# Kernel optimization log

Measured on AMD Instinct MI355X. Metric: run time of the kernel, lower is better.

Reference implementation:

```python
import jax, jax.numpy as jnp
import numpy as np

N_NODES = 100000


def setup_inputs() -> dict:
    key = jax.random.key(0)
    k1, k2, k3 = jax.random.split(key, 3)
    x = jax.random.normal(k1, (N_NODES, 128), dtype=jnp.float32)
    edge_index = jax.random.randint(k2, (2, 1600000), 0, N_NODES, dtype=jnp.int64)
    # TAGConv K=1 linear weight: maps concat([x, Ax]) (2*in) -> out; stored as [(K+1)*in, out]
    W = (jax.random.normal(k3, (256, 128), dtype=jnp.float32) / np.sqrt(256.0)).astype(jnp.float32)
    return {"x": x, "edge_index": edge_index, "W": W}


def reference(x, edge_index, W):
    src, dst = edge_index[0], edge_index[1]
    n = x.shape[0]
    ones = jnp.ones(src.shape[0], dtype=x.dtype)
    # gcn_norm without self-loops: degree from edge weights scattered at target
    deg = jax.ops.segment_sum(ones, dst, num_segments=n)
    dis = jnp.where(deg > 0, jax.lax.rsqrt(jnp.where(deg > 0, deg, 1.0)), 0.0)
    norm = dis[src] * dis[dst]  # [E]
    # message passing: out[dst] += norm * x[src]
    msgs = x[src] * norm[:, None]  # [E, in]
    agg = jax.ops.segment_sum(msgs, dst, num_segments=n)  # [N, in]
    h = jnp.concatenate([x, agg], axis=1)  # [N, 2*in]
    return h @ W  # [N, out]
```

## Files before the change

### kernel.cpp

```cpp
#include <hip/hip_runtime.h>


#define GCN_F 128
#define BINCAP 9216
#define EPACK_ROWS 14112

typedef __attribute__((ext_vector_type(8))) short frag_ab;
typedef __attribute__((ext_vector_type(4))) float frag_cd;

__device__ __forceinline__ unsigned short f2bf(float f) {
    unsigned int u = __float_as_uint(f);
    unsigned int r = (u + 0x7FFFu + ((u >> 16) & 1u)) >> 16;
    return (unsigned short)r;
}

__device__ __forceinline__ int detect_is32(const unsigned int* ei32, int* s_is32) {
    if (threadIdx.x == 0) *s_is32 = 0;
    __syncthreads();
    unsigned int v = 0;
    for (int i = threadIdx.x; i < 2048; i += blockDim.x) v |= ei32[2 * i + 1];
    if (v != 0u) atomicOr(s_is32, 1);
    __syncthreads();
    return *s_is32;
}

__device__ __forceinline__ int load_idx(const int* ei, int is32, long long pos) {
    if (is32) return ei[pos];
    return ((const int2*)ei)[pos].x;
}

__device__ __forceinline__ void xbf_store(const float4* x4, char* xb, int xs, int g) {
    int r = g >> 5, q = g & 31;
    float4 v = x4[(long long)r * 32 + q];
    ushort4 o;
    o.x = f2bf(v.x); o.y = f2bf(v.y); o.z = f2bf(v.z); o.w = f2bf(v.w);
    *(ushort4*)(xb + ((unsigned)r << xs) + q * 8) = o;
}

__global__ __launch_bounds__(256) void bscatter_kernel(const int* __restrict__ ei,
                                                       int* __restrict__ gcur,
                                                       unsigned int* __restrict__ epack,
                                                       int E, int EB,
                                                       const float* __restrict__ W,
                                                       unsigned short* __restrict__ wt,
                                                       const float4* __restrict__ x4,
                                                       char* __restrict__ xb,
                                                       int xs, int g0, int Ntot) {
    int tid = threadIdx.x;
    if ((int)blockIdx.x >= EB + 128) {
        int g = g0 + (blockIdx.x - (EB + 128)) * 256 + tid;
        if (g < Ntot * 32) xbf_store(x4, xb, xs, g);
        return;
    }
    if ((int)blockIdx.x >= EB) {
        int c = blockIdx.x - EB;
        wt[c * 256 + tid] = f2bf(W[tid * GCN_F + c]);
        return;
    }
    __shared__ int h[4][256];
    __shared__ int lcur[256];
    __shared__ int s_is32;
    int wv = tid >> 6;
    for (int i = tid; i < 1024; i += 256) ((int*)h)[i] = 0;
    int is32 = detect_is32((const unsigned int*)ei, &s_is32);
    int base = blockIdx.x * 4096;
    unsigned int pk[16];
    int bn[16];
#pragma unroll
    for (int j = 0; j < 16; ++j) {
        int e = base + j * 256 + tid;
        bn[j] = -1;
        pk[j] = 0;
        if (e < E) {
            int src = load_idx(ei, is32, e);
            int dst = load_idx(ei, is32, (long long)E + e);
            pk[j] = (unsigned int)src | (((unsigned int)dst & 511u) << 17);
            bn[j] = dst >> 9;
            atomicAdd(&h[wv][bn[j]], 1);
        }
    }
    __syncthreads();
    {
        int cnt = h[0][tid] + h[1][tid] + h[2][tid] + h[3][tid];
        if (cnt > 0) {
            int run = atomicAdd(&gcur[tid], cnt);
            if (run + cnt > BINCAP) run = BINCAP - cnt;
            lcur[tid] = tid * BINCAP + run;
        }
    }
    __syncthreads();
#pragma unroll
    for (int j = 0; j < 16; ++j) {
        if (bn[j] >= 0) {
            int pos = atomicAdd(&lcur[bn[j]], 1);
            epack[pos] = pk[j];
        }
    }
}

__global__ __launch_bounds__(512) void fcsr_kernel(const unsigned int* __restrict__ epack,
                                                   const int* __restrict__ gcur,
                                                   int* __restrict__ start,
                                                   float* __restrict__ dis,
                                                   int* __restrict__ ebuf,
                                                   int N) {
    __shared__ int stmp[256];
    __shared__ int s_base, s_total;
    __shared__ int lh[512];
    __shared__ int sc[512];
    int c = blockIdx.x;
    int tid = threadIdx.x;
    int v0 = 0;
    if (tid < 256) {
        v0 = min(gcur[tid], BINCAP);
        stmp[tid] = v0;
    }
    lh[tid] = 0;
    __syncthreads();
    for (int off = 1; off < 256; off <<= 1) {
        int t = (tid < 256 && tid >= off) ? stmp[tid - off] : 0;
        __syncthreads();
        if (tid < 256) stmp[tid] += t;
        __syncthreads();
    }
    if (tid == c) s_base = stmp[tid] - v0;
    if (tid == 255) s_total = stmp[255];
    __syncthreads();
    int b = c * BINCAP;
    int e = b + min(gcur[c], BINCAP);
    for (int i = b + tid; i < e; i += 512) {
        atomicAdd(&lh[(epack[i] >> 17) & 511u], 1);
    }
    __syncthreads();
    sc[tid] = lh[tid];
    __syncthreads();
    for (int off = 1; off < 512; off <<= 1) {
        int t = (tid >= off) ? sc[tid - off] : 0;
        __syncthreads();
        sc[tid] += t;
        __syncthreads();
    }
    int d = lh[tid];
    int gs = s_base + sc[tid] - d;
    int node = c * 512 + tid;
    if (node < N) {
        start[node] = gs;
        dis[node] = (d > 0) ? rsqrtf((float)d) : 0.0f;
    }
    __syncthreads();
    sc[tid] = gs;
    if (c == 0 && tid == 0) start[N] = s_total;
    __syncthreads();
    for (int i = b + tid; i < e; i += 512) {
        unsigned int v = epack[i];
        int pos = atomicAdd(&sc[(v >> 17) & 511u], 1);
        ebuf[pos] = (int)(v & 0x1FFFFu);
    }
}

__global__ __launch_bounds__(256) void xbf_lo_kernel(const float4* __restrict__ x4,
                                                     char* __restrict__ xb, int xs) {
    int g = blockIdx.x * 256 + threadIdx.x;
    if (g >= EPACK_ROWS * 32) return;
    xbf_store(x4, xb, xs, g);
}

__global__ __launch_bounds__(256) void gather_kernel(const char* __restrict__ xb, int xs,
                                                     char* __restrict__ aggb,
                                                     const int* __restrict__ ebuf,
                                                     const int* __restrict__ start,
                                                     const float* __restrict__ dis,
                                                     int N) {
    int node = blockIdx.x * 4 + (threadIdx.x >> 6);
    if (node >= N) return;
    int lane = threadIdx.x & 63;
    int slot = lane >> 4;
    unsigned int subb = (lane & 15) * 16;
    int s = start[node];
    int d = start[node + 1] - s;
    float nd = dis[node];
    float acc[8];
#pragma unroll
    for (int i = 0; i < 8; ++i) acc[i] = 0.0f;

    for (int base = 0; base < d; base += 64) {
        int cn = min(64, d - base);
        int eid = 0; float dv = 0.0f;
        if (lane < cn) {
            eid = ebuf[s + base + lane];
            dv = dis[eid];
        }
        int njj = (cn + 3) >> 2;
#pragma unroll 4
        for (int j = 0; j < njj; ++j) {
            int tt = 4 * j + slot;
            int src = __shfl(eid, tt);
            float f = __shfl(dv, tt);
            uint4 u = *(const uint4*)(xb + (((unsigned)src << xs) + subb));
            acc[0] += f * __uint_as_float(u.x << 16);
            acc[1] += f * __uint_as_float(u.x);
            acc[2] += f * __uint_as_float(u.y << 16);
            acc[3] += f * __uint_as_float(u.y);
            acc[4] += f * __uint_as_float(u.z << 16);
            acc[5] += f * __uint_as_float(u.z);
            acc[6] += f * __uint_as_float(u.w << 16);
            acc[7] += f * __uint_as_float(u.w);
        }
    }
#pragma unroll
    for (int i = 0; i < 8; ++i) {
        acc[i] += __shfl_xor(acc[i], 16);
        acc[i] += __shfl_xor(acc[i], 32);
    }
    if (slot == 0) {
        uint4 o;
        o.x = (unsigned int)f2bf(acc[0] * nd) | ((unsigned int)f2bf(acc[1] * nd) << 16);
        o.y = (unsigned int)f2bf(acc[2] * nd) | ((unsigned int)f2bf(acc[3] * nd) << 16);
        o.z = (unsigned int)f2bf(acc[4] * nd) | ((unsigned int)f2bf(acc[5] * nd) << 16);
        o.w = (unsigned int)f2bf(acc[6] * nd) | ((unsigned int)f2bf(acc[7] * nd) << 16);
        *(uint4*)(aggb + (((unsigned)node << 9) + 256 + subb)) = o;
    }
}

#define GEMM_BM 128
__global__ __launch_bounds__(256) void gemm_mfma_kernel(
        const char* __restrict__ xb, int xs,
        const char* aggb,
        const unsigned short* __restrict__ wt,
        float* out, int N) {
    int wave = threadIdx.x >> 6;
    int lane = threadIdx.x & 63;
    int lr = lane & 15;
    int kh = lane >> 4;
    int rowbase = blockIdx.x * GEMM_BM + wave * 32;

    frag_cd acc[2][8];
#pragma unroll
    for (int rt = 0; rt < 2; ++rt)
#pragma unroll
        for (int ct = 0; ct < 8; ++ct) acc[rt][ct] = (frag_cd)0.0f;

#pragma unroll
    for (int ks = 0; ks < 8; ++ks) {
        frag_ab a[2];
#pragma unroll
        for (int rt = 0; rt < 2; ++rt) {
            int r = rowbase + rt * 16 + lr;
            r = min(r, N - 1);
            const char* ap = (ks < 4)
                ? (xb   + (((unsigned)r << xs) + (unsigned)(ks * 64 + kh * 16)))
                : (aggb + (((unsigned)r << 9) + (unsigned)(256 + (ks - 4) * 64 + kh * 16)));
            a[rt] = *(const frag_ab*)ap;
        }
#pragma unroll
        for (int ct = 0; ct < 8; ++ct) {
            int c = ct * 16 + lr;
            frag_ab b = *(const frag_ab*)(wt + c * 256 + ks * 32 + kh * 8);
#pragma unroll
            for (int rt = 0; rt < 2; ++rt) {
                acc[rt][ct] = __builtin_amdgcn_mfma_f32_16x16x32_bf16(a[rt], b, acc[rt][ct], 0, 0, 0);
            }
        }
    }
#pragma unroll
    for (int rt = 0; rt < 2; ++rt) {
#pragma unroll
        for (int ct = 0; ct < 8; ++ct) {
#pragma unroll
            for (int reg = 0; reg < 4; ++reg) {
                int r = rowbase + rt * 16 + kh * 4 + reg;
                if (r < N) out[r * GCN_F + ct * 16 + lr] = acc[rt][ct][reg];
            }
        }
    }
}

extern "C" void kernel_launch(void* const* d_in, const int* in_sizes, int n_in,
                              void* d_out, int out_size, void* d_ws, size_t ws_size,
                              hipStream_t stream) {
    const float* x  = (const float*)d_in[0];
    const int*   ei = (const int*)d_in[1];
    const float* W  = (const float*)d_in[2];
    float* out = (float*)d_out;

    const int N = in_sizes[0] / GCN_F;
    const int E = in_sizes[1] / 2;

    char* ws = (char*)d_ws;
    int*   gcur  = (int*)ws;
    float* dis   = (float*)(ws + 8192);
    int*   start = (int*)(ws + 408192);
    int*   ebuf  = (int*)(ws + 808208);
    unsigned short* wt = (unsigned short*)(ws + 7208208);
    char*  xb_ws = ws + 7274496;

    unsigned int* epack = (unsigned int*)d_out;
    char*         aggb  = (char*)d_out;

    const size_t WS_NEED = 7274496 + (size_t)N * 256;
    const bool bigws = ws_size >= WS_NEED;

    char* xb = bigws ? xb_ws : (char*)d_out;
    int   xs = bigws ? 8 : 9;
    int g0 = bigws ? 0 : EPACK_ROWS * 32;
    int XR = (N * 32 - g0 + 255) / 256;

    const int CB = (N + 511) / 512;
    const int EB = (E + 4095) / 4096;

    hipMemsetAsync(d_ws, 0, 1024, stream);

    bscatter_kernel<<<EB + 128 + XR, 256, 0, stream>>>(
        ei, gcur, epack, E, EB, W, wt, (const float4*)x, xb, xs, g0, N);
    fcsr_kernel<<<CB, 512, 0, stream>>>(epack, gcur, start, dis, ebuf, N);
    if (!bigws) {
        xbf_lo_kernel<<<(EPACK_ROWS * 32 + 255) / 256, 256, 0, stream>>>(
            (const float4*)x, xb, xs);
    }
    gather_kernel<<<(N + 3) / 4, 256, 0, stream>>>(xb, xs, aggb, ebuf, start, dis, N);
    gemm_mfma_kernel<<<(N + GEMM_BM - 1) / GEMM_BM, 256, 0, stream>>>(
        xb, xs, aggb, wt, out, N);
}
```

Measured before the change: 160.8 us.

## Vectorize edge loads, drop second LDS atomic pass, gather two nodes per wave

```diff
diff --git a/kernel.cpp b/kernel.cpp
--- a/kernel.cpp
+++ b/kernel.cpp
@@ -58,44 +58,84 @@
         return;
     }
     __shared__ int h[4][256];
-    __shared__ int lcur[256];
     __shared__ int s_is32;
     int wv = tid >> 6;
     for (int i = tid; i < 1024; i += 256) ((int*)h)[i] = 0;
     int is32 = detect_is32((const unsigned int*)ei, &s_is32);
     int base = blockIdx.x * 4096;
     unsigned int pk[16];
-    int bn[16];
+    int bn[16], rk[16];
+#pragma unroll
+    for (int j = 0; j < 16; ++j) bn[j] = -1;
+
+#define BS_PROC(j, sv, dv_)                                          \
+    {                                                                \
+        unsigned int ud = (unsigned int)(dv_);                       \
+        pk[j] = (unsigned int)(sv) | ((ud & 511u) << 17);            \
+        int b_ = (int)(ud >> 9);                                     \
+        bn[j] = b_;                                                  \
+        rk[j] = atomicAdd(&h[wv][b_], 1);                            \
+    }
+
+    if (is32 && ((E & 3) == 0)) {
+#pragma unroll
+        for (int jj = 0; jj < 4; ++jj) {
+            int e0 = base + jj * 1024 + tid * 4;
+            if (e0 < E) {
+                int4 s4 = *(const int4*)(ei + e0);
+                int4 d4 = *(const int4*)(ei + (size_t)E + e0);
+                int js = jj * 4;
+                BS_PROC(js + 0, s4.x, d4.x); BS_PROC(js + 1, s4.y, d4.y);
+                BS_PROC(js + 2, s4.z, d4.z); BS_PROC(js + 3, s4.w, d4.w);
+            }
+        }
+    } else if (!is32) {
+#pragma unroll
+        for (int jj = 0; jj < 8; ++jj) {
+            int e0 = base + jj * 512 + tid * 2;
+            if (e0 + 1 < E) {
+                int4 s2 = *(const int4*)((const int2*)ei + e0);
+                int4 d2 = *(const int4*)((const int2*)ei + (size_t)E + e0);
+                BS_PROC(jj * 2 + 0, s2.x, d2.x);
+                BS_PROC(jj * 2 + 1, s2.z, d2.z);
+            } else if (e0 < E) {
+                int sv = ((const int2*)ei)[e0].x;
+                int dv_ = ((const int2*)ei)[(size_t)E + e0].x;
+                BS_PROC(jj * 2, sv, dv_);
+            }
+        }
+    } else {
+        for (int j = 0; j < 16; ++j) {
+            int e = base + j * 256 + tid;
+            if (e < E) {
+                int sv = load_idx(ei, is32, e);
+                int dv_ = load_idx(ei, is32, (long long)E + e);
+                BS_PROC(j, sv, dv_);
+            }
+        }
+    }
+    __syncthreads();
+    {
+        int b = tid;
+        int c0 = h[0][b], c1 = h[1][b], c2 = h[2][b], c3 = h[3][b];
+        int tot = c0 + c1 + c2 + c3;
+        int gbase = 0;
+        if (tot > 0) {
+            gbase = atomicAdd(&gcur[b], tot);
+            if (gbase + tot > BINCAP) gbase = BINCAP - tot;
+        }
+        int p = b * BINCAP + gbase;
+        h[0][b] = p;
+        h[1][b] = p + c0;
+        h[2][b] = p + c0 + c1;
+        h[3][b] = p + c0 + c1 + c2;
+    }
+    __syncthreads();
 #pragma unroll
     for (int j = 0; j < 16; ++j) {
-        int e = base + j * 256 + tid;
-        bn[j] = -1;
-        pk[j] = 0;
-        if (e < E) {
-            int src = load_idx(ei, is32, e);
-            int dst = load_idx(ei, is32, (long long)E + e);
-            pk[j] = (unsigned int)src | (((unsigned int)dst & 511u) << 17);
-            bn[j] = dst >> 9;
-            atomicAdd(&h[wv][bn[j]], 1);
-        }
-    }
-    __syncthreads();
-    {
-        int cnt = h[0][tid] + h[1][tid] + h[2][tid] + h[3][tid];
-        if (cnt > 0) {
-            int run = atomicAdd(&gcur[tid], cnt);
-            if (run + cnt > BINCAP) run = BINCAP - cnt;
-            lcur[tid] = tid * BINCAP + run;
-        }
-    }
-    __syncthreads();
-#pragma unroll
-    for (int j = 0; j < 16; ++j) {
-        if (bn[j] >= 0) {
-            int pos = atomicAdd(&lcur[bn[j]], 1);
-            epack[pos] = pk[j];
-        }
-    }
+        if (bn[j] >= 0) epack[h[wv][bn[j]] + rk[j]] = pk[j];
+    }
+#undef BS_PROC
 }
 
 __global__ __launch_bounds__(512) void fcsr_kernel(const unsigned int* __restrict__ epack,
@@ -171,54 +211,85 @@
                                                      const int* __restrict__ start,
                                                      const float* __restrict__ dis,
                                                      int N) {
-    int node = blockIdx.x * 4 + (threadIdx.x >> 6);
-    if (node >= N) return;
+    int wv = threadIdx.x >> 6;
+    int n0 = blockIdx.x * 8 + wv * 2;
+    if (n0 >= N) return;
     int lane = threadIdx.x & 63;
     int slot = lane >> 4;
     unsigned int subb = (lane & 15) * 16;
-    int s = start[node];
-    int d = start[node + 1] - s;
-    float nd = dis[node];
-    float acc[8];
-#pragma unroll
-    for (int i = 0; i < 8; ++i) acc[i] = 0.0f;
-
-    for (int base = 0; base < d; base += 64) {
-        int cn = min(64, d - base);
-        int eid = 0; float dv = 0.0f;
-        if (lane < cn) {
-            eid = ebuf[s + base + lane];
-            dv = dis[eid];
-        }
-        int njj = (cn + 3) >> 2;
+    bool two = (n0 + 1) < N;
+    int s0 = start[n0];
+    int m0 = start[n0 + 1];
+    int d0 = m0 - s0;
+    int s1 = m0;
+    int d1 = two ? (start[n0 + 2] - m0) : 0;
+    float nd0 = dis[n0];
+    float nd1 = two ? dis[n0 + 1] : 0.0f;
+    float a0[8], a1[8];
+#pragma unroll
+    for (int i = 0; i < 8; ++i) { a0[i] = 0.0f; a1[i] = 0.0f; }
+
+    int dmax = max(d0, d1);
+    for (int base = 0; base < dmax; base += 64) {
+        int cn0 = min(64, max(0, d0 - base));
+        int cn1 = min(64, max(0, d1 - base));
+        int eid0 = 0, eid1 = 0;
+        float dv0 = 0.0f, dv1 = 0.0f;
+        if (lane < cn0) { eid0 = ebuf[s0 + base + lane]; dv0 = dis[eid0]; }
+        if (lane < cn1) { eid1 = ebuf[s1 + base + lane]; dv1 = dis[eid1]; }
+        int njj = (max(cn0, cn1) + 3) >> 2;
 #pragma unroll 4
         for (int j = 0; j < njj; ++j) {
             int tt = 4 * j + slot;
-            int src = __shfl(eid, tt);
-            float f = __shfl(dv, tt);
-            uint4 u = *(const uint4*)(xb + (((unsigned)src << xs) + subb));
-            acc[0] += f * __uint_as_float(u.x << 16);
-            acc[1] += f * __uint_as_float(u.x);
-            acc[2] += f * __uint_as_float(u.y << 16);
-            acc[3] += f * __uint_as_float(u.y);
-            acc[4] += f * __uint_as_float(u.z << 16);
-            acc[5] += f * __uint_as_float(u.z);
-            acc[6] += f * __uint_as_float(u.w << 16);
-            acc[7] += f * __uint_as_float(u.w);
+            int sr0 = __shfl(eid0, tt);
+            float f0 = __shfl(dv0, tt);
+            int sr1 = __shfl(eid1, tt);
+            float f1 = __shfl(dv1, tt);
+            if (tt < cn0) {
+                uint4 u = *(const uint4*)(xb + (((unsigned)sr0 << xs) + subb));
+                a0[0] += f0 * __uint_as_float(u.x << 16);
+                a0[1] += f0 * __uint_as_float(u.x);
+                a0[2] += f0 * __uint_as_float(u.y << 16);
+                a0[3] += f0 * __uint_as_float(u.y);
+                a0[4] += f0 * __uint_as_float(u.z << 16);
+                a0[5] += f0 * __uint_as_float(u.z);
+                a0[6] += f0 * __uint_as_float(u.w << 16);
+                a0[7] += f0 * __uint_as_float(u.w);
+            }
+            if (tt < cn1) {
+                uint4 u = *(const uint4*)(xb + (((unsigned)sr1 << xs) + subb));
+                a1[0] += f1 * __uint_as_float(u.x << 16);
+                a1[1] += f1 * __uint_as_float(u.x);
+                a1[2] += f1 * __uint_as_float(u.y << 16);
+                a1[3] += f1 * __uint_as_float(u.y);
+                a1[4] += f1 * __uint_as_float(u.z << 16);
+                a1[5] += f1 * __uint_as_float(u.z);
+                a1[6] += f1 * __uint_as_float(u.w << 16);
+                a1[7] += f1 * __uint_as_float(u.w);
+            }
         }
     }
 #pragma unroll
     for (int i = 0; i < 8; ++i) {
-        acc[i] += __shfl_xor(acc[i], 16);
-        acc[i] += __shfl_xor(acc[i], 32);
+        a0[i] += __shfl_xor(a0[i], 16);
+        a0[i] += __shfl_xor(a0[i], 32);
+        a1[i] += __shfl_xor(a1[i], 16);
+        a1[i] += __shfl_xor(a1[i], 32);
     }
     if (slot == 0) {
         uint4 o;
-        o.x = (unsigned int)f2bf(acc[0] * nd) | ((unsigned int)f2bf(acc[1] * nd) << 16);
-        o.y = (unsigned int)f2bf(acc[2] * nd) | ((unsigned int)f2bf(acc[3] * nd) << 16);
-        o.z = (unsigned int)f2bf(acc[4] * nd) | ((unsigned int)f2bf(acc[5] * nd) << 16);
-        o.w = (unsigned int)f2bf(acc[6] * nd) | ((unsigned int)f2bf(acc[7] * nd) << 16);
-        *(uint4*)(aggb + (((unsigned)node << 9) + 256 + subb)) = o;
+        o.x = (unsigned int)f2bf(a0[0] * nd0) | ((unsigned int)f2bf(a0[1] * nd0) << 16);
+        o.y = (unsigned int)f2bf(a0[2] * nd0) | ((unsigned int)f2bf(a0[3] * nd0) << 16);
+        o.z = (unsigned int)f2bf(a0[4] * nd0) | ((unsigned int)f2bf(a0[5] * nd0) << 16);
+        o.w = (unsigned int)f2bf(a0[6] * nd0) | ((unsigned int)f2bf(a0[7] * nd0) << 16);
+        *(uint4*)(aggb + (((unsigned)n0 << 9) + 256 + subb)) = o;
+    } else if (slot == 1 && two) {
+        uint4 o;
+        o.x = (unsigned int)f2bf(a1[0] * nd1) | ((unsigned int)f2bf(a1[1] * nd1) << 16);
+        o.y = (unsigned int)f2bf(a1[2] * nd1) | ((unsigned int)f2bf(a1[3] * nd1) << 16);
+        o.z = (unsigned int)f2bf(a1[4] * nd1) | ((unsigned int)f2bf(a1[5] * nd1) << 16);
+        o.w = (unsigned int)f2bf(a1[6] * nd1) | ((unsigned int)f2bf(a1[7] * nd1) << 16);
+        *(uint4*)(aggb + ((((unsigned)n0 + 1u) << 9) + 256 + subb)) = o;
     }
 }
 
@@ -317,7 +388,7 @@
         xbf_lo_kernel<<<(EPACK_ROWS * 32 + 255) / 256, 256, 0, stream>>>(
             (const float4*)x, xb, xs);
     }
-    gather_kernel<<<(N + 3) / 4, 256, 0, stream>>>(xb, xs, aggb, ebuf, start, dis, N);
+    gather_kernel<<<(N + 7) / 8, 256, 0, stream>>>(xb, xs, aggb, ebuf, start, dis, N);
     gemm_mfma_kernel<<<(N + GEMM_BM - 1) / GEMM_BM, 256, 0, stream>>>(
         xb, xs, aggb, wt, out, N);
 }
```

Result: no change. 160.2 us (-0.4%).

## Use finer 128-node bins, vectorized edge loads, and per-wave rank offsets in CSR build

Applied to the files above, without the earlier changes.

```diff
diff --git a/kernel.cpp b/kernel.cpp
--- a/kernel.cpp
+++ b/kernel.cpp
@@ -2,8 +2,8 @@
 
 
 #define GCN_F 128
-#define BINCAP 9216
-#define EPACK_ROWS 14112
+#define BINCAP 2560
+#define EPACK_ROWS 15640
 
 typedef __attribute__((ext_vector_type(8))) short frag_ab;
 typedef __attribute__((ext_vector_type(4))) float frag_cd;
@@ -40,7 +40,7 @@
 __global__ __launch_bounds__(256) void bscatter_kernel(const int* __restrict__ ei,
                                                        int* __restrict__ gcur,
                                                        unsigned int* __restrict__ epack,
-                                                       int E, int EB,
+                                                       int E, int EB, int nb,
                                                        const float* __restrict__ W,
                                                        unsigned short* __restrict__ wt,
                                                        const float4* __restrict__ x4,
@@ -57,103 +57,136 @@
         wt[c * 256 + tid] = f2bf(W[tid * GCN_F + c]);
         return;
     }
-    __shared__ int h[4][256];
-    __shared__ int lcur[256];
+    __shared__ int h[4][800];
     __shared__ int s_is32;
     int wv = tid >> 6;
-    for (int i = tid; i < 1024; i += 256) ((int*)h)[i] = 0;
+    for (int i = tid; i < 4 * 800; i += 256) ((int*)h)[i] = 0;
     int is32 = detect_is32((const unsigned int*)ei, &s_is32);
     int base = blockIdx.x * 4096;
     unsigned int pk[16];
-    int bn[16];
+    int bn[16], rk[16];
+#pragma unroll
+    for (int j = 0; j < 16; ++j) bn[j] = -1;
+
+#define BS_PROC(j, sv, dv_)                                          \
+    {                                                                \
+        unsigned int ud = (unsigned int)(dv_);                       \
+        pk[j] = (unsigned int)(sv) | ((ud & 127u) << 17);            \
+        int b_ = (int)(ud >> 7);                                     \
+        bn[j] = b_;                                                  \
+        rk[j] = atomicAdd(&h[wv][b_], 1);                            \
+    }
+
+    if (is32 && ((E & 3) == 0)) {
+#pragma unroll
+        for (int jj = 0; jj < 4; ++jj) {
+            int e0 = base + jj * 1024 + tid * 4;
+            if (e0 < E) {
+                int4 s4 = *(const int4*)(ei + e0);
+                int4 d4 = *(const int4*)(ei + (size_t)E + e0);
+                int js = jj * 4;
+                BS_PROC(js + 0, s4.x, d4.x); BS_PROC(js + 1, s4.y, d4.y);
+                BS_PROC(js + 2, s4.z, d4.z); BS_PROC(js + 3, s4.w, d4.w);
+            }
+        }
+    } else if (!is32) {
+#pragma unroll
+        for (int jj = 0; jj < 8; ++jj) {
+            int e0 = base + jj * 512 + tid * 2;
+            if (e0 + 1 < E) {
+                int4 s2 = *(const int4*)((const int2*)ei + e0);
+                int4 d2 = *(const int4*)((const int2*)ei + (size_t)E + e0);
+                BS_PROC(jj * 2 + 0, s2.x, d2.x);
+                BS_PROC(jj * 2 + 1, s2.z, d2.z);
+            } else if (e0 < E) {
+                int sv = ((const int2*)ei)[e0].x;
+                int dv_ = ((const int2*)ei)[(size_t)E + e0].x;
+                BS_PROC(jj * 2, sv, dv_);
+            }
+        }
+    } else {
+        for (int j = 0; j < 16; ++j) {
+            int e = base + j * 256 + tid;
+            if (e < E) {
+                int sv = load_idx(ei, is32, e);
+                int dv_ = load_idx(ei, is32, (long long)E + e);
+                BS_PROC(j, sv, dv_);
+            }
+        }
+    }
+    __syncthreads();
+    for (int b = tid; b < nb; b += 256) {
+        int c0 = h[0][b], c1 = h[1][b], c2 = h[2][b], c3 = h[3][b];
+        int tot = c0 + c1 + c2 + c3;
+        int gbase = 0;
+        if (tot > 0) {
+            gbase = atomicAdd(&gcur[b], tot);
+            if (gbase + tot > BINCAP) gbase = BINCAP - tot;
+        }
+        int p = b * BINCAP + gbase;
+        h[0][b] = p;
+        h[1][b] = p + c0;
+        h[2][b] = p + c0 + c1;
+        h[3][b] = p + c0 + c1 + c2;
+    }
+    __syncthreads();
 #pragma unroll
     for (int j = 0; j < 16; ++j) {
-        int e = base + j * 256 + tid;
-        bn[j] = -1;
-        pk[j] = 0;
-        if (e < E) {
-            int src = load_idx(ei, is32, e);
-            int dst = load_idx(ei, is32, (long long)E + e);
-            pk[j] = (unsigned int)src | (((unsigned int)dst & 511u) << 17);
-            bn[j] = dst >> 9;
-            atomicAdd(&h[wv][bn[j]], 1);
-        }
-    }
-    __syncthreads();
-    {
-        int cnt = h[0][tid] + h[1][tid] + h[2][tid] + h[3][tid];
-        if (cnt > 0) {
-            int run = atomicAdd(&gcur[tid], cnt);
-            if (run + cnt > BINCAP) run = BINCAP - cnt;
-            lcur[tid] = tid * BINCAP + run;
-        }
-    }
-    __syncthreads();
-#pragma unroll
-    for (int j = 0; j < 16; ++j) {
-        if (bn[j] >= 0) {
-            int pos = atomicAdd(&lcur[bn[j]], 1);
-            epack[pos] = pk[j];
-        }
-    }
-}
-
-__global__ __launch_bounds__(512) void fcsr_kernel(const unsigned int* __restrict__ epack,
+        if (bn[j] >= 0) epack[h[wv][bn[j]] + rk[j]] = pk[j];
+    }
+#undef BS_PROC
+}
+
+__global__ __launch_bounds__(256) void fcsr_kernel(const unsigned int* __restrict__ epack,
                                                    const int* __restrict__ gcur,
                                                    int* __restrict__ start,
                                                    float* __restrict__ dis,
                                                    int* __restrict__ ebuf,
-                                                   int N) {
-    __shared__ int stmp[256];
-    __shared__ int s_base, s_total;
-    __shared__ int lh[512];
-    __shared__ int sc[512];
+                                                   int N, int E) {
+    __shared__ int red[256];
+    __shared__ int lh[128];
+    __shared__ int sc[128];
     int c = blockIdx.x;
     int tid = threadIdx.x;
-    int v0 = 0;
-    if (tid < 256) {
-        v0 = min(gcur[tid], BINCAP);
-        stmp[tid] = v0;
-    }
-    lh[tid] = 0;
-    __syncthreads();
-    for (int off = 1; off < 256; off <<= 1) {
-        int t = (tid < 256 && tid >= off) ? stmp[tid - off] : 0;
+    int partial = 0;
+    for (int b = tid; b < c; b += 256) partial += min(gcur[b], BINCAP);
+    red[tid] = partial;
+    if (tid < 128) lh[tid] = 0;
+    __syncthreads();
+    for (int off = 128; off > 0; off >>= 1) {
+        if (tid < off) red[tid] += red[tid + off];
         __syncthreads();
-        if (tid < 256) stmp[tid] += t;
+    }
+    int s_base = red[0];
+    int b0 = c * BINCAP;
+    int e0 = b0 + min(gcur[c], BINCAP);
+    for (int i = b0 + tid; i < e0; i += 256) {
+        atomicAdd(&lh[(epack[i] >> 17) & 127u], 1);
+    }
+    __syncthreads();
+    if (tid < 128) sc[tid] = lh[tid];
+    __syncthreads();
+    for (int off = 1; off < 128; off <<= 1) {
+        int t = (tid < 128 && tid >= off) ? sc[tid - off] : 0;
         __syncthreads();
-    }
-    if (tid == c) s_base = stmp[tid] - v0;
-    if (tid == 255) s_total = stmp[255];
-    __syncthreads();
-    int b = c * BINCAP;
-    int e = b + min(gcur[c], BINCAP);
-    for (int i = b + tid; i < e; i += 512) {
-        atomicAdd(&lh[(epack[i] >> 17) & 511u], 1);
-    }
-    __syncthreads();
-    sc[tid] = lh[tid];
-    __syncthreads();
-    for (int off = 1; off < 512; off <<= 1) {
-        int t = (tid >= off) ? sc[tid - off] : 0;
+        if (tid < 128) sc[tid] += t;
         __syncthreads();
-        sc[tid] += t;
-        __syncthreads();
-    }
-    int d = lh[tid];
-    int gs = s_base + sc[tid] - d;
-    int node = c * 512 + tid;
-    if (node < N) {
-        start[node] = gs;
-        dis[node] = (d > 0) ? rsqrtf((float)d) : 0.0f;
-    }
-    __syncthreads();
-    sc[tid] = gs;
-    if (c == 0 && tid == 0) start[N] = s_total;
-    __syncthreads();
-    for (int i = b + tid; i < e; i += 512) {
+    }
+    if (tid < 128) {
+        int d = lh[tid];
+        int gs = s_base + sc[tid] - d;
+        int node = c * 128 + tid;
+        if (node < N) {
+            start[node] = gs;
+            dis[node] = (d > 0) ? rsqrtf((float)d) : 0.0f;
+        }
+        sc[tid] = gs;
+    }
+    if (c == 0 && tid == 0) start[N] = E;
+    __syncthreads();
+    for (int i = b0 + tid; i < e0; i += 256) {
         unsigned int v = epack[i];
-        int pos = atomicAdd(&sc[(v >> 17) & 511u], 1);
+        int pos = atomicAdd(&sc[(v >> 17) & 127u], 1);
         ebuf[pos] = (int)(v & 0x1FFFFu);
     }
 }
@@ -305,14 +338,14 @@
     int g0 = bigws ? 0 : EPACK_ROWS * 32;
     int XR = (N * 32 - g0 + 255) / 256;
 
-    const int CB = (N + 511) / 512;
+    const int NB = (N + 127) / 128;
     const int EB = (E + 4095) / 4096;
 
-    hipMemsetAsync(d_ws, 0, 1024, stream);
+    hipMemsetAsync(d_ws, 0, 4096, stream);
 
     bscatter_kernel<<<EB + 128 + XR, 256, 0, stream>>>(
-        ei, gcur, epack, E, EB, W, wt, (const float4*)x, xb, xs, g0, N);
-    fcsr_kernel<<<CB, 512, 0, stream>>>(epack, gcur, start, dis, ebuf, N);
+        ei, gcur, epack, E, EB, NB, W, wt, (const float4*)x, xb, xs, g0, N);
+    fcsr_kernel<<<NB, 256, 0, stream>>>(epack, gcur, start, dis, ebuf, N, E);
     if (!bigws) {
         xbf_lo_kernel<<<(EPACK_ROWS * 32 + 255) / 256, 256, 0, stream>>>(
             (const float4*)x, xb, xs);
```

Result: no change. 158.8 us, median of 2 (-1.2%).
